# Performance work log

Measured on AMD Instinct MI355X. Metric: run time of the kernel, lower is better.

Reference implementation:

```python
import jax, jax.numpy as jnp
import numpy as np
import math

# ---- static config (must match init_kwargs / input_specs) ----
D = 1024
N_HEAD = 16
HEAD_DIM = D // N_HEAD          # 64
HALF = HEAD_DIM // 2            # rope half dim = 32
N_EXP = 8
TOP_K = 2
CAP_FACTOR = 2.0
LN_EPS = 1e-5


def _build_sin_cos(T, half_dim, dtype=jnp.float32):
    pos = jnp.arange(T, dtype=dtype)[:, None]                      # (T,1)
    inv_freq = 1.0 / (10000.0 ** (jnp.arange(0, 2 * half_dim, 2, dtype=dtype) / (2 * half_dim)))
    ang = pos * inv_freq[None, :]                                  # (T, half)
    return jnp.sin(ang), jnp.cos(ang)


def _layernorm(x, g, b):
    mu = jnp.mean(x, axis=-1, keepdims=True)
    var = jnp.mean(jnp.square(x - mu), axis=-1, keepdims=True)
    return (x - mu) * jax.lax.rsqrt(var + LN_EPS) * g + b


def _apply_rope(q, k, sin, cos):
    # q,k: (B,T,H,hd); sin,cos: (T, half)
    s = sin[None, :, None, :]
    c = cos[None, :, None, :]
    q1, q2 = q[..., :HALF], q[..., HALF:]
    k1, k2 = k[..., :HALF], k[..., HALF:]
    qr = jnp.concatenate([q1 * c - q2 * s, q1 * s + q2 * c], axis=-1)
    kr = jnp.concatenate([k1 * c - k2 * s, k1 * s + k2 * c], axis=-1)
    return qr, kr


def _attention(x, Wqkv, Wproj):
    B, T, C = x.shape
    qkv = x @ Wqkv                                                  # (B,T,3C)
    qkv = qkv.reshape(B, T, N_HEAD, 3 * HEAD_DIM)
    q, k, v = jnp.split(qkv, 3, axis=-1)                            # each (B,T,H,hd)
    sin, cos = _build_sin_cos(T, HALF)
    q, k = _apply_rope(q, k, sin, cos)
    scale = 1.0 / math.sqrt(HEAD_DIM)
    att = jnp.einsum('bqhd,bkhd->bhqk', q, k) * scale               # (B,H,T,T)
    causal = jnp.tril(jnp.ones((T, T), dtype=bool))
    att = jnp.where(causal[None, None], att, jnp.finfo(att.dtype).min)
    p = jax.nn.softmax(att, axis=-1)
    o = jnp.einsum('bhqk,bkhd->bqhd', p, v).reshape(B, T, C)
    return o @ Wproj, k, v


def _sparse_moe(flat, Wgate, W1, b1, W2, b2):
    # flat: (N, d). Eval mode: no router noise.
    N, d = flat.shape
    capacity = int(math.ceil(CAP_FACTOR * N / N_EXP))
    logits = flat @ Wgate                                           # (N,E)
    gates = jax.nn.softmax(logits, axis=-1)
    vals, inds = jax.lax.top_k(gates, TOP_K)                        # (N,k)
    flat_inds = inds.reshape(-1)                                    # (N*k,)
    flat_vals = vals.reshape(-1)
    neg = jnp.finfo(flat.dtype).min
    # per-expert assignment scores over all (token, slot) pairs
    scores = jnp.where(flat_inds[None, :] == jnp.arange(N_EXP)[:, None],
                       flat_vals[None, :], neg)                     # (E, N*k)
    top_scores, top_pos = jax.lax.top_k(scores, capacity)           # (E, cap)
    tok_idx = top_pos // TOP_K                                      # (E, cap)
    w = jnp.where(top_scores > neg, top_scores, 0.0)                # dropped slots -> 0 weight
    xe = flat[tok_idx]                                              # gather: (E, cap, d)
    h = jax.nn.gelu(jnp.einsum('ecd,edh->ech', xe, W1) + b1[:, None, :], approximate=False)
    out = jnp.einsum('ech,ehd->ecd', h, W2) + b2[:, None, :]
    out = out * w[..., None]
    final = jnp.zeros_like(flat).at[tok_idx.reshape(-1)].add(out.reshape(-1, d))
    return final


def setup_inputs() -> dict:
    key = jax.random.key(0)
    ks = jax.random.split(key, 10)
    B, T = 2, 2048
    s = 0.02
    return {
        'x': jax.random.normal(ks[0], (B, T, D), dtype=jnp.float32),
        'ln1_g': jnp.ones((D,), jnp.float32),
        'ln1_b': jnp.zeros((D,), jnp.float32),
        'ln2_g': jnp.ones((D,), jnp.float32),
        'ln2_b': jnp.zeros((D,), jnp.float32),
        'Wqkv': jax.random.normal(ks[1], (D, 3 * D), jnp.float32) * s,
        'Wproj': jax.random.normal(ks[2], (D, D), jnp.float32) * s,
        'Wgate': jax.random.normal(ks[3], (D, N_EXP), jnp.float32) * s,
        'W1': jax.random.normal(ks[4], (N_EXP, D, 4 * D), jnp.float32) * s,
        'b1': jnp.zeros((N_EXP, 4 * D), jnp.float32),
        'W2': jax.random.normal(ks[5], (N_EXP, 4 * D, D), jnp.float32) * s,
        'b2': jnp.zeros((N_EXP, D), jnp.float32),
    }


def reference(x, ln1_g, ln1_b, ln2_g, ln2_b, Wqkv, Wproj, Wgate, W1, b1, W2, b2):
    B, T, _ = x.shape
    x_norm = _layernorm(x, ln1_g, ln1_b)
    attn_out, k, v = _attention(x_norm, Wqkv, Wproj)
    x = x + attn_out
    ff_in = _layernorm(x, ln2_g, ln2_b)
    moe_out = _sparse_moe(ff_in.reshape(B * T, D), Wgate, W1, b1, W2, b2)
    x = x + moe_out.reshape(B, T, D)
    aux_loss = jnp.zeros((), x.dtype)  # eval mode
    return x, aux_loss, k, v
```

## Files before the change

### kernel.cpp

```cpp
#include <hip/hip_runtime.h>
#include <hip/hip_bf16.h>
#include <math.h>


#define TT 2048
#define NTOK 4096

typedef __attribute__((ext_vector_type(8))) short bf16x8;
typedef __attribute__((ext_vector_type(4))) float f32x4;
typedef __attribute__((ext_vector_type(16))) float f32x16;

static __device__ __forceinline__ ushort f2bf(float f) {
  union { float f; unsigned u; } v; v.f = f;
  unsigned r = v.u + 0x7FFFu + ((v.u >> 16) & 1u);
  return (ushort)(r >> 16);
}
static __device__ __forceinline__ float bf2f(ushort h) {
  union { unsigned u; float f; } v; v.u = ((unsigned)h) << 16; return v.f;
}
static __device__ __forceinline__ unsigned cvt_pk_bf16(float lo, float hi) {
  unsigned r;
  asm("v_cvt_pk_bf16_f32 %0, %1, %2" : "=v"(r) : "v"(lo), "v"(hi));
  return r;
}
static __device__ __forceinline__ void plane_swap(unsigned& a, unsigned& b) {
  asm("v_permlane32_swap_b32 %0, %1" : "+v"(a), "+v"(b));
}

__global__ __launch_bounds__(256)
void ln_kernel(const float* __restrict__ x, const float* __restrict__ g,
               const float* __restrict__ b, float* __restrict__ out) {
  int row = blockIdx.x, tid = threadIdx.x;
  const float4* xr = (const float4*)(x + (size_t)row * 1024);
  float4 v = xr[tid];
  float s = v.x + v.y + v.z + v.w;
  #pragma unroll
  for (int off = 1; off < 64; off <<= 1) s += __shfl_xor(s, off);
  __shared__ float red1[4], red2[4];
  if ((tid & 63) == 0) red1[tid >> 6] = s;
  __syncthreads();
  float mu = (red1[0] + red1[1] + red1[2] + red1[3]) * (1.0f / 1024.0f);
  float dx = v.x - mu, dy = v.y - mu, dz = v.z - mu, dw = v.w - mu;
  float ss = dx*dx + dy*dy + dz*dz + dw*dw;
  #pragma unroll
  for (int off = 1; off < 64; off <<= 1) ss += __shfl_xor(ss, off);
  if ((tid & 63) == 0) red2[tid >> 6] = ss;
  __syncthreads();
  float var = (red2[0] + red2[1] + red2[2] + red2[3]) * (1.0f / 1024.0f);
  float inv = 1.0f / sqrtf(var + 1e-5f);
  float4 g4 = ((const float4*)g)[tid];
  float4 b4 = ((const float4*)b)[tid];
  float4 o4;
  o4.x = dx * inv * g4.x + b4.x;
  o4.y = dy * inv * g4.y + b4.y;
  o4.z = dz * inv * g4.z + b4.z;
  o4.w = dw * inv * g4.w + b4.w;
  ((float4*)(out + (size_t)row * 1024))[tid] = o4;
}

__global__ void sincos_kernel(float* __restrict__ st, float* __restrict__ ct) {
  int t = blockIdx.x, j = threadIdx.x;
  double invf = pow(10000.0, -((double)(2 * j)) / 64.0);
  double ang = (double)t * invf;
  st[t * 32 + j] = (float)sin(ang);
  ct[t * 32 + j] = (float)cos(ang);
}

__global__ __launch_bounds__(256)
void rope_kernel(float* __restrict__ qkv, const float* __restrict__ st,
                 const float* __restrict__ ct, float* __restrict__ kout,
                 float* __restrict__ vout, ushort* __restrict__ Kh,
                 ushort* __restrict__ Kl) {
  int row = blockIdx.x;
  int t = row & (TT - 1);
  int b = row >> 11;
  int tid = threadIdx.x;
  float* base = qkv + (size_t)row * 3072;
  #pragma unroll
  for (int l = 0; l < 2; ++l) {
    int idx = l * 256 + tid;
    int h = idx >> 5, j = idx & 31;
    float s = st[t * 32 + j], c = ct[t * 32 + j];
    float* qp = base + h * 192;
    float q1 = qp[j], q2 = qp[j + 32];
    qp[j]      = q1 * c - q2 * s;
    qp[j + 32] = q1 * s + q2 * c;
    float k1 = qp[64 + j], k2 = qp[96 + j];
    float kr1 = k1 * c - k2 * s, kr2 = k1 * s + k2 * c;
    qp[64 + j] = kr1; qp[96 + j] = kr2;
    kout[(size_t)row * 1024 + h * 64 + j]      = kr1;
    kout[(size_t)row * 1024 + h * 64 + 32 + j] = kr2;
    size_t kb = ((size_t)(b * 16 + h) * TT + t) * 64;
    ushort h1 = f2bf(kr1);
    Kh[kb + j] = h1; Kl[kb + j] = f2bf(kr1 - bf2f(h1));
    ushort h2 = f2bf(kr2);
    Kh[kb + 32 + j] = h2; Kl[kb + 32 + j] = f2bf(kr2 - bf2f(h2));
  }
  #pragma unroll
  for (int l = 0; l < 4; ++l) {
    int f = l * 256 + tid;
    int h = f >> 6, d = f & 63;
    vout[(size_t)row * 1024 + f] = base[h * 192 + 128 + d];
  }
}

__global__ __launch_bounds__(256)
void vtprep_kernel(const float* __restrict__ vout, ushort* __restrict__ Vth,
                   ushort* __restrict__ Vtl) {
  __shared__ float tile[64][65];
  int t0 = blockIdx.x * 64, h = blockIdx.y, b = blockIdx.z;
  int tid = threadIdx.x;
  #pragma unroll
  for (int l = 0; l < 4; ++l) {
    int idx = l * 256 + tid;
    int r = idx >> 4, c4 = (idx & 15) * 4;
    *(float4*)&tile[r][c4] = *(const float4*)&vout[((size_t)(b * TT + t0 + r)) * 1024 + h * 64 + c4];
  }
  __syncthreads();
  int d = tid >> 2, ts = (tid & 3) * 16;
  union { bf16x8 v; ushort u[8]; } H0, H1, L0, L1;
  #pragma unroll
  for (int i = 0; i < 8; ++i) {
    float v0 = tile[ts + i][d];
    ushort hb0 = f2bf(v0);
    H0.u[i] = hb0; L0.u[i] = f2bf(v0 - bf2f(hb0));
    float v1 = tile[ts + 8 + i][d];
    ushort hb1 = f2bf(v1);
    H1.u[i] = hb1; L1.u[i] = f2bf(v1 - bf2f(hb1));
  }
  size_t basep = ((size_t)(b * 16 + h) * 64 + d) * TT + t0 + ts;
  *(bf16x8*)(Vth + basep) = H0.v;  *(bf16x8*)(Vth + basep + 8) = H1.v;
  *(bf16x8*)(Vtl + basep) = L0.v;  *(bf16x8*)(Vtl + basep + 8) = L1.v;
}

__global__ __launch_bounds__(256)
void flash6_kernel(const float* __restrict__ qkv, const ushort* __restrict__ Kh,
                   const ushort* __restrict__ Kl, const ushort* __restrict__ Vth,
                   const ushort* __restrict__ Vtl, float* __restrict__ Opart,
                   float* __restrict__ Mpart, float* __restrict__ Lpart) {
  int lin = blockIdx.x;
  int xcd = lin & 7, s = lin >> 3;
  int bh = xcd + 8 * (s / 40);
  int j = 39 - (s % 40);
  int qt, kc;
  if (j < 4)       { qt = j;                    kc = 0; }
  else if (j < 12) { qt = 4 + ((j - 4) >> 1);   kc = (j - 4) & 1; }
  else if (j < 24) { qt = 8 + (j - 12) / 3;     kc = (j - 12) % 3; }
  else             { qt = 12 + ((j - 24) >> 2); kc = (j - 24) & 3; }
  int slot = bh * 40 + j;
  int h = bh & 15, b = bh >> 4;
  int tid = threadIdx.x;
  int w = tid >> 6, lane = tid & 63;
  int q = lane & 31, LH = lane >> 5;
  size_t bT = (size_t)b * TT;
  int qglob0 = qt * 128 + w * 32;
  int qg = qglob0 + q;
  bf16x8 qH[4], qL[4];
  {
    const float* qp = qkv + (bT + qg) * 3072 + h * 192 + LH * 8;
    #pragma unroll
    for (int dblk = 0; dblk < 4; ++dblk) {
      float4 f0 = *(const float4*)(qp + dblk * 16);
      float4 f1 = *(const float4*)(qp + dblk * 16 + 4);
      float vals[8] = {f0.x, f0.y, f0.z, f0.w, f1.x, f1.y, f1.z, f1.w};
      union { bf16x8 v; ushort u[8]; } H, L;
      #pragma unroll
      for (int e = 0; e < 8; ++e) {
        ushort hb = f2bf(vals[e]);
        H.u[e] = hb; L.u[e] = f2bf(vals[e] - bf2f(hb));
      }
      qH[dblk] = H.v; qL[dblk] = L.v;
    }
  }
  const ushort* Kbh = Kh + (size_t)bh * TT * 64;
  const ushort* Kbl = Kl + (size_t)bh * TT * 64;
  const ushort* Vbh = Vth + (size_t)bh * 64 * TT;
  const ushort* Vbl = Vtl + (size_t)bh * 64 * TT;
  f32x16 accO0 = {}, accO1 = {};
  float m = -3.402823466e38f, lsum = 0.0f;
  int kvlo = kc * 512;
  int kvhi = min(kc * 512 + 512, qglob0 + 32);

  for (int kv0 = kvlo; kv0 < kvhi; kv0 += 32) {
    const ushort* kbh = Kbh + (size_t)(kv0 + q) * 64 + LH * 8;
    const ushort* kbl = Kbl + (size_t)(kv0 + q) * 64 + LH * 8;
    bf16x8 kAH[4], kAL[4];
    #pragma unroll
    for (int dblk = 0; dblk < 4; ++dblk) {
      kAH[dblk] = *(const bf16x8*)(kbh + dblk * 16);
      kAL[dblk] = *(const bf16x8*)(kbl + dblk * 16);
    }
    f32x16 sa = {}, sb = {};
    sa = __builtin_amdgcn_mfma_f32_32x32x16_bf16(kAH[0], qH[0], sa, 0, 0, 0);
    sb = __builtin_amdgcn_mfma_f32_32x32x16_bf16(kAH[2], qH[2], sb, 0, 0, 0);
    sa = __builtin_amdgcn_mfma_f32_32x32x16_bf16(kAH[1], qH[1], sa, 0, 0, 0);
    sb = __builtin_amdgcn_mfma_f32_32x32x16_bf16(kAH[3], qH[3], sb, 0, 0, 0);
    sa = __builtin_amdgcn_mfma_f32_32x32x16_bf16(kAH[0], qL[0], sa, 0, 0, 0);
    sb = __builtin_amdgcn_mfma_f32_32x32x16_bf16(kAH[2], qL[2], sb, 0, 0, 0);
    sa = __builtin_amdgcn_mfma_f32_32x32x16_bf16(kAH[1], qL[1], sa, 0, 0, 0);
    sb = __builtin_amdgcn_mfma_f32_32x32x16_bf16(kAH[3], qL[3], sb, 0, 0, 0);
    sa = __builtin_amdgcn_mfma_f32_32x32x16_bf16(kAL[0], qH[0], sa, 0, 0, 0);
    sb = __builtin_amdgcn_mfma_f32_32x32x16_bf16(kAL[2], qH[2], sb, 0, 0, 0);
    sa = __builtin_amdgcn_mfma_f32_32x32x16_bf16(kAL[1], qH[1], sa, 0, 0, 0);
    sb = __builtin_amdgcn_mfma_f32_32x32x16_bf16(kAL[3], qH[3], sb, 0, 0, 0);
    bf16x8 vAH[2][2], vAL[2][2];
    #pragma unroll
    for (int dblk = 0; dblk < 2; ++dblk)
      #pragma unroll
      for (int s2 = 0; s2 < 2; ++s2) {
        size_t ad = (size_t)(dblk * 32 + q) * TT + kv0 + s2 * 16 + LH * 8;
        vAH[dblk][s2] = *(const bf16x8*)(Vbh + ad);
        vAL[dblk][s2] = *(const bf16x8*)(Vbl + ad);
      }
    float p[16];
    float pmax = -3.402823466e38f;
    if (kv0 + 31 > qglob0) {
      #pragma unroll
      for (int r = 0; r < 16; ++r) {
        int kvg = kv0 + (r & 3) + 8 * (r >> 2) + 4 * LH;
        float sv = (kvg <= qg) ? (sa[r] + sb[r]) * 0.125f : -3.402823466e38f;
        p[r] = sv; pmax = fmaxf(pmax, sv);
      }
    } else {
      #pragma unroll
      for (int r = 0; r < 16; ++r) {
        float sv = (sa[r] + sb[r]) * 0.125f;
        p[r] = sv; pmax = fmaxf(pmax, sv);
      }
    }
    pmax = fmaxf(pmax, __shfl_xor(pmax, 32));
    float mnew = fmaxf(m, pmax);
    float fsc = __expf(m - mnew);
    float psum = 0.0f;
    #pragma unroll
    for (int r = 0; r < 16; ++r) { p[r] = __expf(p[r] - mnew); psum += p[r]; }
    psum += __shfl_xor(psum, 32);
    lsum = lsum * fsc + psum;
    m = mnew;
    #pragma unroll
    for (int r = 0; r < 16; ++r) { accO0[r] *= fsc; accO1[r] *= fsc; }
    bf16x8 pHf[2], pLf[2];
    #pragma unroll
    for (int s2 = 0; s2 < 2; ++s2) {
      int s8 = s2 * 8;
      unsigned a  = cvt_pk_bf16(p[s8 + 0], p[s8 + 1]);
      unsigned bw = cvt_pk_bf16(p[s8 + 2], p[s8 + 3]);
      unsigned c  = cvt_pk_bf16(p[s8 + 4], p[s8 + 5]);
      unsigned d  = cvt_pk_bf16(p[s8 + 6], p[s8 + 7]);
      float l0 = p[s8 + 0] - __uint_as_float(a << 16);
      float l1 = p[s8 + 1] - __uint_as_float(a & 0xFFFF0000u);
      float l2 = p[s8 + 2] - __uint_as_float(bw << 16);
      float l3 = p[s8 + 3] - __uint_as_float(bw & 0xFFFF0000u);
      float l4 = p[s8 + 4] - __uint_as_float(c << 16);
      float l5 = p[s8 + 5] - __uint_as_float(c & 0xFFFF0000u);
      float l6 = p[s8 + 6] - __uint_as_float(d << 16);
      float l7 = p[s8 + 7] - __uint_as_float(d & 0xFFFF0000u);
      unsigned al = cvt_pk_bf16(l0, l1);
      unsigned bl = cvt_pk_bf16(l2, l3);
      unsigned cl = cvt_pk_bf16(l4, l5);
      unsigned dl = cvt_pk_bf16(l6, l7);
      plane_swap(a, c); plane_swap(bw, d);
      plane_swap(al, cl); plane_swap(bl, dl);
      union { unsigned w[4]; bf16x8 v; } PH, PL;
      PH.w[0] = a;  PH.w[1] = bw; PH.w[2] = c;  PH.w[3] = d;
      PL.w[0] = al; PL.w[1] = bl; PL.w[2] = cl; PL.w[3] = dl;
      pHf[s2] = PH.v; pLf[s2] = PL.v;
    }
    #pragma unroll
    for (int s2 = 0; s2 < 2; ++s2) {
      accO0 = __builtin_amdgcn_mfma_f32_32x32x16_bf16(vAH[0][s2], pHf[s2], accO0, 0, 0, 0);
      accO1 = __builtin_amdgcn_mfma_f32_32x32x16_bf16(vAH[1][s2], pHf[s2], accO1, 0, 0, 0);
      accO0 = __builtin_amdgcn_mfma_f32_32x32x16_bf16(vAH[0][s2], pLf[s2], accO0, 0, 0, 0);
      accO1 = __builtin_amdgcn_mfma_f32_32x32x16_bf16(vAH[1][s2], pLf[s2], accO1, 0, 0, 0);
      accO0 = __builtin_amdgcn_mfma_f32_32x32x16_bf16(vAL[0][s2], pHf[s2], accO0, 0, 0, 0);
      accO1 = __builtin_amdgcn_mfma_f32_32x32x16_bf16(vAL[1][s2], pHf[s2], accO1, 0, 0, 0);
    }
  }
  if (LH == 0) {
    Mpart[slot * 128 + w * 32 + q] = m;
    Lpart[slot * 128 + w * 32 + q] = lsum;
  }
  float* Ob = Opart + (size_t)slot * 8192 + (w * 32 + q) * 64;
  #pragma unroll
  for (int g2 = 0; g2 < 4; ++g2) {
    float4 v0 = {accO0[g2 * 4 + 0], accO0[g2 * 4 + 1], accO0[g2 * 4 + 2], accO0[g2 * 4 + 3]};
    *(float4*)(Ob + 8 * g2 + 4 * LH) = v0;
    float4 v1 = {accO1[g2 * 4 + 0], accO1[g2 * 4 + 1], accO1[g2 * 4 + 2], accO1[g2 * 4 + 3]};
    *(float4*)(Ob + 32 + 8 * g2 + 4 * LH) = v1;
  }
}

__global__ __launch_bounds__(256)
void fmerge2_kernel(const float* __restrict__ Opart, const float* __restrict__ Mpart,
                    const float* __restrict__ Lpart, float* __restrict__ o) {
  int qt = blockIdx.x, bh = blockIdx.y;
  int h = bh & 15, b = bh >> 4;
  int g = qt >> 2;
  int nc = g + 1;
  int off = 2 * g * (g + 1) + (qt & 3) * (g + 1);
  int slot0 = bh * 40 + off;
  int tid = threadIdx.x;
  int q = tid & 127, dh = tid >> 7;
  float mg = -3.402823466e38f;
  for (int c = 0; c < nc; ++c) mg = fmaxf(mg, Mpart[(slot0 + c) * 128 + q]);
  float lg = 0.0f;
  float4 acc[8] = {};
  for (int c = 0; c < nc; ++c) {
    float sc = __expf(Mpart[(slot0 + c) * 128 + q] - mg);
    lg += sc * Lpart[(slot0 + c) * 128 + q];
    const float4* op = (const float4*)(Opart + (size_t)(slot0 + c) * 8192 + q * 64 + dh * 32);
    #pragma unroll
    for (int i = 0; i < 8; ++i) {
      float4 v = op[i];
      acc[i].x += sc * v.x; acc[i].y += sc * v.y;
      acc[i].z += sc * v.z; acc[i].w += sc * v.w;
    }
  }
  float inv = 1.0f / lg;
  float* ob = o + ((size_t)(b * TT + qt * 128 + q)) * 1024 + h * 64 + dh * 32;
  #pragma unroll
  for (int i = 0; i < 8; ++i) {
    float4 v = {acc[i].x * inv, acc[i].y * inv, acc[i].z * inv, acc[i].w * inv};
    *(float4*)(ob + i * 4) = v;
  }
}

template<bool LO>
__global__ void tconv_kernel(const float* __restrict__ in, ushort* __restrict__ oh,
                             ushort* __restrict__ ol, int K, int N) {
  __shared__ float t[32][33];
  int z = blockIdx.z;
  const float* ip = in + (size_t)z * K * N;
  ushort* ohp = oh + (size_t)z * K * N;
  ushort* olp = LO ? (ol + (size_t)z * K * N) : nullptr;
  int n0 = blockIdx.x * 32, k0 = blockIdx.y * 32;
  int tx = threadIdx.x, ty = threadIdx.y;
  #pragma unroll
  for (int i = 0; i < 4; ++i)
    t[ty + 8 * i][tx] = ip[(size_t)(k0 + ty + 8 * i) * N + n0 + tx];
  __syncthreads();
  #pragma unroll
  for (int i = 0; i < 4; ++i) {
    float v = t[tx][ty + 8 * i];
    size_t off = (size_t)(n0 + ty + 8 * i) * K + k0 + tx;
    ushort hb = f2bf(v);
    ohp[off] = hb;
    if (LO) olp[off] = f2bf(v - bf2f(hb));
  }
}

__global__ __launch_bounds__(256)
void split_kernel(const float* __restrict__ in, ushort* __restrict__ oh,
                  ushort* __restrict__ ol) {
  size_t i = ((size_t)blockIdx.x * 256 + threadIdx.x) * 4;
  float4 v = *(const float4*)(in + i);
  ushort h0 = f2bf(v.x), h1 = f2bf(v.y), h2 = f2bf(v.z), h3 = f2bf(v.w);
  ushort4 hh = {h0, h1, h2, h3};
  *(ushort4*)(oh + i) = hh;
  ushort4 ll = {f2bf(v.x - bf2f(h0)), f2bf(v.y - bf2f(h1)),
                f2bf(v.z - bf2f(h2)), f2bf(v.w - bf2f(h3))};
  *(ushort4*)(ol + i) = ll;
}

#define LOAD_STEP(tt) do {                                                     \
    int seg = SPLIT3 ? ((tt) / kPer) : 0;                                      \
    int kk = (SPLIT3 ? ((tt) % kPer) : (tt)) << 6;                             \
    const ushort* Ause = (SPLIT3 && seg == 2) ? AlB : AhB;                     \
    const ushort* Buse = (SPLIT3 && seg == 1) ? BlB : BhB;                     \
    _Pragma("unroll")                                                          \
    for (int q = 0; q < 4; ++q) {                                              \
      int rr = r0 + 32 * q;                                                    \
      int clog = cph ^ (rr & 7);                                               \
      ra[q] = *(const bf16x8*)(Ause + (size_t)garow[q] * K + kk + clog * 8);   \
      rb[q] = *(const bf16x8*)(Buse + (size_t)(bn + rr) * K + kk + clog * 8);  \
    }                                                                          \
  } while (0)

template<int EPI, bool GATHER, bool SPLIT3>
__global__ __launch_bounds__(256, 2)
void mgemm(const ushort* __restrict__ Ah, const ushort* __restrict__ Al,
           const ushort* __restrict__ Bh, const ushort* __restrict__ Bl,
           void* __restrict__ Cv, const float* __restrict__ extra,
           const int* __restrict__ gatAll, int N, int K,
           long aEStride, long bEStride, long cEStride, int biasEStride) {
  __shared__ ushort As[128 * 64];
  __shared__ ushort Bs[128 * 64];
  int z = blockIdx.z;
  const ushort* AhB = Ah + (size_t)z * aEStride;
  const ushort* AlB = SPLIT3 ? (Al + (size_t)z * aEStride) : nullptr;
  const ushort* BhB = Bh + (size_t)z * bEStride;
  const ushort* BlB = SPLIT3 ? (Bl + (size_t)z * bEStride) : nullptr;
  const int* gat = GATHER ? (gatAll + z * 1024) : nullptr;
  int bm = blockIdx.y * 128, bn = blockIdx.x * 128;
  int tid = threadIdx.x;
  int r0 = tid >> 3, cph = tid & 7;
  int garow[4];
  #pragma unroll
  for (int q = 0; q < 4; ++q) {
    int rr = r0 + 32 * q;
    garow[q] = GATHER ? gat[bm + rr] : (bm + rr);
  }
  int kPer = K >> 6;
  int kSteps = (SPLIT3 ? 3 : 1) * kPer;
  int wid = tid >> 6, lane = tid & 63;
  int wm = wid >> 1, wn = wid & 1;
  int lr = lane & 15, lk = lane >> 4;
  f32x4 acc[4][4] = {};
  bf16x8 ra[4], rb[4];
  LOAD_STEP(0);
  for (int t = 0; t < kSteps; ++t) {
    __syncthreads();
    #pragma unroll
    for (int q = 0; q < 4; ++q) {
      int rr = r0 + 32 * q;
      *(bf16x8*)&As[rr * 64 + cph * 8] = ra[q];
      *(bf16x8*)&Bs[rr * 64 + cph * 8] = rb[q];
    }
    __syncthreads();
    if (t + 1 < kSteps) LOAD_STEP(t + 1);
    #pragma unroll
    for (int kh = 0; kh < 2; ++kh) {
      bf16x8 af[4], bfr[4];
      #pragma unroll
      for (int mf = 0; mf < 4; ++mf) {
        int row = wm * 64 + mf * 16 + lr;
        int ch = (kh * 4 + lk) ^ (row & 7);
        af[mf] = *(const bf16x8*)&As[row * 64 + ch * 8];
      }
      #pragma unroll
      for (int nf = 0; nf < 4; ++nf) {
        int row = wn * 64 + nf * 16 + lr;
        int ch = (kh * 4 + lk) ^ (row & 7);
        bfr[nf] = *(const bf16x8*)&Bs[row * 64 + ch * 8];
      }
      #pragma unroll
      for (int mf = 0; mf < 4; ++mf)
        #pragma unroll
        for (int nf = 0; nf < 4; ++nf)
          acc[mf][nf] = __builtin_amdgcn_mfma_f32_16x16x32_bf16(af[mf], bfr[nf], acc[mf][nf], 0, 0, 0);
    }
  }
  int crow = bm + wm * 64, ccol = bn + wn * 64;
  if constexpr (EPI <= 1) {
    float* C = (float*)Cv;
    #pragma unroll
    for (int mf = 0; mf < 4; ++mf)
      #pragma unroll
      for (int nf = 0; nf < 4; ++nf)
        #pragma unroll
        for (int r = 0; r < 4; ++r) {
          int row = crow + mf * 16 + lk * 4 + r;
          int col = ccol + nf * 16 + lr;
          float v = acc[mf][nf][r];
          if constexpr (EPI == 1) v += extra[(size_t)row * N + col];
          C[(size_t)row * N + col] = v;
        }
  } else {
    const float* bias = extra + (size_t)z * biasEStride;
    ushort* C = (ushort*)Cv + (size_t)z * cEStride;
    #pragma unroll
    for (int mf = 0; mf < 4; ++mf)
      #pragma unroll
      for (int nf = 0; nf < 4; ++nf)
        #pragma unroll
        for (int r = 0; r < 4; ++r) {
          int row = crow + mf * 16 + lk * 4 + r;
          int col = ccol + nf * 16 + lr;
          float v = acc[mf][nf][r] + bias[col];
          if constexpr (EPI == 2)
            v = 0.5f * v * (1.0f + erff(v * 0.70710678118654752f));
          C[(size_t)row * N + col] = f2bf(v);
        }
  }
}

__global__ __launch_bounds__(256)
void gate_kernel(const float* __restrict__ ffin, const float* __restrict__ Wg,
                 int* __restrict__ te, float* __restrict__ tv, int* __restrict__ inv) {
  int token = blockIdx.x, tid = threadIdx.x;
  float acc[8] = {};
  const float* xr = ffin + (size_t)token * 1024;
  for (int i = tid; i < 1024; i += 256) {
    float xv = xr[i];
    const float4* wr = (const float4*)&Wg[i * 8];
    float4 w0 = wr[0], w1 = wr[1];
    acc[0] += xv * w0.x; acc[1] += xv * w0.y; acc[2] += xv * w0.z; acc[3] += xv * w0.w;
    acc[4] += xv * w1.x; acc[5] += xv * w1.y; acc[6] += xv * w1.z; acc[7] += xv * w1.w;
  }
  #pragma unroll
  for (int off = 1; off < 64; off <<= 1)
    #pragma unroll
    for (int q = 0; q < 8; ++q) acc[q] += __shfl_xor(acc[q], off);
  __shared__ float red[4][8];
  if ((tid & 63) == 0)
    #pragma unroll
    for (int q = 0; q < 8; ++q) red[tid >> 6][q] = acc[q];
  __syncthreads();
  if (tid == 0) {
    float g[8];
    #pragma unroll
    for (int q = 0; q < 8; ++q) g[q] = red[0][q] + red[1][q] + red[2][q] + red[3][q];
    float mx = g[0];
    #pragma unroll
    for (int q = 1; q < 8; ++q) mx = fmaxf(mx, g[q]);
    float sum = 0.0f;
    #pragma unroll
    for (int q = 0; q < 8; ++q) { g[q] = expf(g[q] - mx); sum += g[q]; }
    float inv_s = 1.0f / sum;
    #pragma unroll
    for (int q = 0; q < 8; ++q) g[q] *= inv_s;
    int e1 = 0; float v1 = g[0];
    for (int q = 1; q < 8; ++q) if (g[q] > v1) { v1 = g[q]; e1 = q; }
    int e2 = -1; float v2 = -1.0f;
    for (int q = 0; q < 8; ++q) { if (q == e1) continue; if (g[q] > v2) { v2 = g[q]; e2 = q; } }
    te[token * 2] = e1; te[token * 2 + 1] = e2;
    tv[token * 2] = v1; tv[token * 2 + 1] = v2;
    inv[token * 2] = -1; inv[token * 2 + 1] = -1;
  }
}

__global__ __launch_bounds__(1024)
void route_sort_kernel(const int* __restrict__ te, const float* __restrict__ tv,
                       int* __restrict__ etok, float* __restrict__ ew,
                       int* __restrict__ inv) {
  __shared__ unsigned long long sk[4096];
  __shared__ int wcnt[16];
  __shared__ int base;
  int e = blockIdx.x, tid = threadIdx.x;
  int lane = tid & 63, wv = tid >> 6;
  if (tid == 0) base = 0;
  __syncthreads();
  for (int c = 0; c < 8; ++c) {
    int s = c * 1024 + tid;
    bool sel = (te[s] == e);
    unsigned long long ball = __ballot(sel);
    int pre = __popcll(ball & ((1ull << lane) - 1ull));
    if (lane == 0) wcnt[wv] = __popcll(ball);
    __syncthreads();
    int woff = 0, tot = 0;
    #pragma unroll
    for (int i = 0; i < 16; ++i) {
      int cc = wcnt[i];
      if (i < wv) woff += cc;
      tot += cc;
    }
    if (sel) {
      unsigned vb = __float_as_uint(tv[s]);
      sk[base + woff + pre] =
          ((unsigned long long)vb << 32) | (unsigned)(0xFFFFFFFFu - (unsigned)s);
    }
    __syncthreads();
    if (tid == 0) base += tot;
    __syncthreads();
  }
  int n = base;
  if (n > 1024) {
    int P = (n <= 2048) ? 2048 : 4096;
    for (int i = n + tid; i < P; i += 1024) sk[i] = 0ull;
    __syncthreads();
    for (int k = 2; k <= P; k <<= 1)
      for (int j = k >> 1; j > 0; j >>= 1) {
        for (int t = tid; t < (P >> 1); t += 1024) {
          int i = ((t & ~(j - 1)) << 1) | (t & (j - 1));
          int p = i | j;
          unsigned long long a = sk[i], bq = sk[p];
          bool desc = ((i & k) == 0);
          if (desc ? (a < bq) : (a > bq)) { sk[i] = bq; sk[p] = a; }
        }
        __syncthreads();
      }
  }
  int cap = n < 1024 ? n : 1024;
  if (tid < cap) {
    unsigned long long key = sk[tid];
    unsigned slot = 0xFFFFFFFFu - (unsigned)(key & 0xFFFFFFFFull);
    etok[e * 1024 + tid] = (int)(slot >> 1);
    ew[e * 1024 + tid] = __uint_as_float((unsigned)(key >> 32));
    inv[slot] = e * 1024 + tid;
  } else {
    etok[e * 1024 + tid] = 0;
    ew[e * 1024 + tid] = 0.0f;
  }
}

__global__ __launch_bounds__(256)
void combine_kernel(const float* __restrict__ xres, const ushort* __restrict__ eo,
                    const int* __restrict__ inv, const float* __restrict__ ew,
                    float* __restrict__ outx, float* __restrict__ aux) {
  int token = blockIdx.x;
  int d = threadIdx.x * 4;
  float4 acc = *(const float4*)&xres[(size_t)token * 1024 + d];
  #pragma unroll
  for (int j = 0; j < 2; ++j) {
    int p = inv[token * 2 + j];
    if (p >= 0) {
      float w = ew[p];
      const ushort* ep = eo + (size_t)p * 1024 + d;
      acc.x += w * bf2f(ep[0]); acc.y += w * bf2f(ep[1]);
      acc.z += w * bf2f(ep[2]); acc.w += w * bf2f(ep[3]);
    }
  }
  *(float4*)&outx[(size_t)token * 1024 + d] = acc;
  if (token == 0 && threadIdx.x == 0) aux[0] = 0.0f;
}

extern "C" void kernel_launch(void* const* d_in, const int* in_sizes, int n_in,
                              void* d_out, int out_size, void* d_ws, size_t ws_size,
                              hipStream_t stream) {
  const float* x     = (const float*)d_in[0];
  const float* ln1g  = (const float*)d_in[1];
  const float* ln1b  = (const float*)d_in[2];
  const float* ln2g  = (const float*)d_in[3];
  const float* ln2b  = (const float*)d_in[4];
  const float* Wqkv  = (const float*)d_in[5];
  const float* Wproj = (const float*)d_in[6];
  const float* Wg    = (const float*)d_in[7];
  const float* W1    = (const float*)d_in[8];
  const float* b1    = (const float*)d_in[9];
  const float* W2    = (const float*)d_in[10];
  const float* b2    = (const float*)d_in[11];

  float* out_x   = (float*)d_out;
  float* out_aux = out_x + 4194304;
  float* out_k   = out_aux + 1;
  float* out_v   = out_k + 4194304;

  float* ws   = (float*)d_ws;
  float* A    = ws;
  float* qkvb = ws + 4194304;
  float* o    = ws + 16777216;
  float* st   = ws + 20971520;
  float* ct   = ws + 21037056;
  int*   te   = (int*)(ws + 21102592);
  float* tv   = ws + 21110784;
  int*   etok = (int*)(ws + 21118976);
  float* ew   = ws + 21127168;
  int*   inv  = (int*)(ws + 21135360);
  ushort* bfAh = (ushort*)(ws + 21143552);
  ushort* bfAl = (ushort*)(ws + 23240704);
  ushort* BqH  = (ushort*)(ws + 25337856);
  ushort* BqL  = (ushort*)(ws + 26910720);
  ushort* BpH  = (ushort*)(ws + 28483584);
  ushort* BpL  = (ushort*)(ws + 29007872);
  ushort* W1t  = (ushort*)(ws + 29532160);
  ushort* W2t  = (ushort*)(ws + 46309376);
  ushort* eo   = (ushort*)(ws + 63086592);
  ushort* hbuf = (ushort*)(ws + 4194304);
  ushort* Kh_  = bfAh;
  ushort* Kl_  = bfAl;
  ushort* Vth_ = eo;
  ushort* Vtl_ = eo + 4194304;
  float* Opart = ws + 29532160;
  float* Mpart = ws + 40017920;
  float* Lpart = ws + 40181760;

  tconv_kernel<true ><<<dim3(96, 32, 1),  dim3(32, 8), 0, stream>>>(Wqkv,  BqH, BqL, 1024, 3072);
  tconv_kernel<true ><<<dim3(32, 32, 1),  dim3(32, 8), 0, stream>>>(Wproj, BpH, BpL, 1024, 1024);
  sincos_kernel<<<TT, 32, 0, stream>>>(st, ct);

  ln_kernel<<<NTOK, 256, 0, stream>>>(x, ln1g, ln1b, A);
  split_kernel<<<4096, 256, 0, stream>>>(A, bfAh, bfAl);
  mgemm<0, false, true><<<dim3(24, 32, 1), 256, 0, stream>>>(
      bfAh, bfAl, BqH, BqL, qkvb, nullptr, nullptr, 3072, 1024, 0, 0, 0, 0);
  rope_kernel<<<NTOK, 256, 0, stream>>>(qkvb, st, ct, out_k, out_v, Kh_, Kl_);
  vtprep_kernel<<<dim3(32, 16, 2), 256, 0, stream>>>(out_v, Vth_, Vtl_);
  flash6_kernel<<<1280, 256, 0, stream>>>(qkvb, Kh_, Kl_, Vth_, Vtl_, Opart, Mpart, Lpart);
  fmerge2_kernel<<<dim3(16, 32), 256, 0, stream>>>(Opart, Mpart, Lpart, o);
  split_kernel<<<4096, 256, 0, stream>>>(o, bfAh, bfAl);
  mgemm<1, false, true><<<dim3(8, 32, 1), 256, 0, stream>>>(
      bfAh, bfAl, BpH, BpL, A, x, nullptr, 1024, 1024, 0, 0, 0, 0);
  tconv_kernel<false><<<dim3(128, 32, 8), dim3(32, 8), 0, stream>>>(W1, W1t, nullptr, 1024, 4096);
  tconv_kernel<false><<<dim3(32, 128, 8), dim3(32, 8), 0, stream>>>(W2, W2t, nullptr, 4096, 1024);
  ln_kernel<<<NTOK, 256, 0, stream>>>(A, ln2g, ln2b, o);
  gate_kernel<<<NTOK, 256, 0, stream>>>(o, Wg, te, tv, inv);
  split_kernel<<<4096, 256, 0, stream>>>(o, bfAh, bfAl);
  route_sort_kernel<<<8, 1024, 0, stream>>>(te, tv, etok, ew, inv);
  mgemm<2, true, false><<<dim3(32, 8, 8), 256, 0, stream>>>(
      bfAh, nullptr, W1t, nullptr, hbuf, b1, etok, 4096, 1024,
      0, 4096L * 1024, 1024L * 4096, 4096);
  mgemm<3, false, false><<<dim3(8, 8, 8), 256, 0, stream>>>(
      hbuf, nullptr, W2t, nullptr, eo, b2, nullptr, 1024, 4096,
      1024L * 4096, 1024L * 4096, 1024L * 1024, 1024);
  combine_kernel<<<NTOK, 256, 0, stream>>>(A, eo, inv, ew, out_x, out_aux);
}
```

Baseline: 699.3 us.

## Fuse bf16 hi/lo split into producers and load GEMM tiles directly to LDS

Removes the three separate split kernels by having the layernorm and flash-merge kernels write bf16 hi/lo pairs directly, which drops an fp32 round trip through global memory for each one. Separately, the mgemm kernel now uses global_load_lds to copy A/B tiles straight into shared memory in place of register staging. The register-prefetch of the next k-step is gone, so global-load latency is no longer overlapped with MFMA work within a block. Overlap now depends on the second resident block per CU.

After: 711.5 us. Within noise of the previous version (+1.7%).

```diff
diff --git a/kernel.cpp b/kernel.cpp
--- a/kernel.cpp
+++ b/kernel.cpp
@@ -26,10 +26,17 @@
 static __device__ __forceinline__ void plane_swap(unsigned& a, unsigned& b) {
   asm("v_permlane32_swap_b32 %0, %1" : "+v"(a), "+v"(b));
 }
-
+static __device__ __forceinline__ void gload16(const void* g, void* l) {
+  __builtin_amdgcn_global_load_lds(
+      (const __attribute__((address_space(1))) void*)g,
+      (__attribute__((address_space(3))) void*)l, 16, 0, 0);
+}
+
+template<bool WF32>
 __global__ __launch_bounds__(256)
 void ln_kernel(const float* __restrict__ x, const float* __restrict__ g,
-               const float* __restrict__ b, float* __restrict__ out) {
+               const float* __restrict__ b, float* __restrict__ out,
+               ushort* __restrict__ oh, ushort* __restrict__ ol) {
   int row = blockIdx.x, tid = threadIdx.x;
   const float4* xr = (const float4*)(x + (size_t)row * 1024);
   float4 v = xr[tid];
@@ -55,7 +62,15 @@
   o4.y = dy * inv * g4.y + b4.y;
   o4.z = dz * inv * g4.z + b4.z;
   o4.w = dw * inv * g4.w + b4.w;
-  ((float4*)(out + (size_t)row * 1024))[tid] = o4;
+  if constexpr (WF32)
+    ((float4*)(out + (size_t)row * 1024))[tid] = o4;
+  size_t base = (size_t)row * 1024 + tid * 4;
+  ushort h0 = f2bf(o4.x), h1 = f2bf(o4.y), h2 = f2bf(o4.z), h3 = f2bf(o4.w);
+  ushort4 hh = {h0, h1, h2, h3};
+  *(ushort4*)(oh + base) = hh;
+  ushort4 ll = {f2bf(o4.x - bf2f(h0)), f2bf(o4.y - bf2f(h1)),
+                f2bf(o4.z - bf2f(h2)), f2bf(o4.w - bf2f(h3))};
+  *(ushort4*)(ol + base) = ll;
 }
 
 __global__ void sincos_kernel(float* __restrict__ st, float* __restrict__ ct) {
@@ -292,7 +307,8 @@
 
 __global__ __launch_bounds__(256)
 void fmerge2_kernel(const float* __restrict__ Opart, const float* __restrict__ Mpart,
-                    const float* __restrict__ Lpart, float* __restrict__ o) {
+                    const float* __restrict__ Lpart, ushort* __restrict__ oh,
+                    ushort* __restrict__ ol) {
   int qt = blockIdx.x, bh = blockIdx.y;
   int h = bh & 15, b = bh >> 4;
   int g = qt >> 2;
@@ -317,11 +333,16 @@
     }
   }
   float inv = 1.0f / lg;
-  float* ob = o + ((size_t)(b * TT + qt * 128 + q)) * 1024 + h * 64 + dh * 32;
+  size_t obase = ((size_t)(b * TT + qt * 128 + q)) * 1024 + h * 64 + dh * 32;
   #pragma unroll
   for (int i = 0; i < 8; ++i) {
     float4 v = {acc[i].x * inv, acc[i].y * inv, acc[i].z * inv, acc[i].w * inv};
-    *(float4*)(ob + i * 4) = v;
+    ushort h0 = f2bf(v.x), h1 = f2bf(v.y), h2 = f2bf(v.z), h3 = f2bf(v.w);
+    ushort4 hh = {h0, h1, h2, h3};
+    *(ushort4*)(oh + obase + i * 4) = hh;
+    ushort4 ll = {f2bf(v.x - bf2f(h0)), f2bf(v.y - bf2f(h1)),
+                  f2bf(v.z - bf2f(h2)), f2bf(v.w - bf2f(h3))};
+    *(ushort4*)(ol + obase + i * 4) = ll;
   }
 }
 
@@ -348,33 +369,6 @@
     if (LO) olp[off] = f2bf(v - bf2f(hb));
   }
 }
-
-__global__ __launch_bounds__(256)
-void split_kernel(const float* __restrict__ in, ushort* __restrict__ oh,
-                  ushort* __restrict__ ol) {
-  size_t i = ((size_t)blockIdx.x * 256 + threadIdx.x) * 4;
-  float4 v = *(const float4*)(in + i);
-  ushort h0 = f2bf(v.x), h1 = f2bf(v.y), h2 = f2bf(v.z), h3 = f2bf(v.w);
-  ushort4 hh = {h0, h1, h2, h3};
-  *(ushort4*)(oh + i) = hh;
-  ushort4 ll = {f2bf(v.x - bf2f(h0)), f2bf(v.y - bf2f(h1)),
-                f2bf(v.z - bf2f(h2)), f2bf(v.w - bf2f(h3))};
-  *(ushort4*)(ol + i) = ll;
-}
-
-#define LOAD_STEP(tt) do {                                                     \
-    int seg = SPLIT3 ? ((tt) / kPer) : 0;                                      \
-    int kk = (SPLIT3 ? ((tt) % kPer) : (tt)) << 6;                             \
-    const ushort* Ause = (SPLIT3 && seg == 2) ? AlB : AhB;                     \
-    const ushort* Buse = (SPLIT3 && seg == 1) ? BlB : BhB;                     \
-    _Pragma("unroll")                                                          \
-    for (int q = 0; q < 4; ++q) {                                              \
-      int rr = r0 + 32 * q;                                                    \
-      int clog = cph ^ (rr & 7);                                               \
-      ra[q] = *(const bf16x8*)(Ause + (size_t)garow[q] * K + kk + clog * 8);   \
-      rb[q] = *(const bf16x8*)(Buse + (size_t)(bn + rr) * K + kk + clog * 8);  \
-    }                                                                          \
-  } while (0)
 
 template<int EPI, bool GATHER, bool SPLIT3>
 __global__ __launch_bounds__(256, 2)
@@ -393,31 +387,35 @@
   const int* gat = GATHER ? (gatAll + z * 1024) : nullptr;
   int bm = blockIdx.y * 128, bn = blockIdx.x * 128;
   int tid = threadIdx.x;
-  int r0 = tid >> 3, cph = tid & 7;
+  int wid = tid >> 6, lane = tid & 63;
+  int w32 = wid * 32;
+  int lrow = lane >> 3, cph = lane & 7;
   int garow[4];
   #pragma unroll
-  for (int q = 0; q < 4; ++q) {
-    int rr = r0 + 32 * q;
-    garow[q] = GATHER ? gat[bm + rr] : (bm + rr);
+  for (int i = 0; i < 4; ++i) {
+    int row = w32 + i * 8 + lrow;
+    garow[i] = GATHER ? gat[bm + row] : (bm + row);
   }
   int kPer = K >> 6;
   int kSteps = (SPLIT3 ? 3 : 1) * kPer;
-  int wid = tid >> 6, lane = tid & 63;
   int wm = wid >> 1, wn = wid & 1;
   int lr = lane & 15, lk = lane >> 4;
   f32x4 acc[4][4] = {};
-  bf16x8 ra[4], rb[4];
-  LOAD_STEP(0);
+
   for (int t = 0; t < kSteps; ++t) {
+    int seg = SPLIT3 ? (t / kPer) : 0;
+    int kk = (SPLIT3 ? (t % kPer) : t) << 6;
+    const ushort* Ause = (SPLIT3 && seg == 2) ? AlB : AhB;
+    const ushort* Buse = (SPLIT3 && seg == 1) ? BlB : BhB;
     __syncthreads();
     #pragma unroll
-    for (int q = 0; q < 4; ++q) {
-      int rr = r0 + 32 * q;
-      *(bf16x8*)&As[rr * 64 + cph * 8] = ra[q];
-      *(bf16x8*)&Bs[rr * 64 + cph * 8] = rb[q];
+    for (int i = 0; i < 4; ++i) {
+      int row = w32 + i * 8 + lrow;
+      int sc = cph ^ (row & 7);
+      gload16(Ause + (size_t)garow[i] * K + kk + sc * 8, As + (w32 + i * 8) * 64);
+      gload16(Buse + (size_t)(bn + row) * K + kk + sc * 8, Bs + (w32 + i * 8) * 64);
     }
     __syncthreads();
-    if (t + 1 < kSteps) LOAD_STEP(t + 1);
     #pragma unroll
     for (int kh = 0; kh < 2; ++kh) {
       bf16x8 af[4], bfr[4];
@@ -658,22 +656,19 @@
   tconv_kernel<true ><<<dim3(32, 32, 1),  dim3(32, 8), 0, stream>>>(Wproj, BpH, BpL, 1024, 1024);
   sincos_kernel<<<TT, 32, 0, stream>>>(st, ct);
 
-  ln_kernel<<<NTOK, 256, 0, stream>>>(x, ln1g, ln1b, A);
-  split_kernel<<<4096, 256, 0, stream>>>(A, bfAh, bfAl);
+  ln_kernel<false><<<NTOK, 256, 0, stream>>>(x, ln1g, ln1b, nullptr, bfAh, bfAl);
   mgemm<0, false, true><<<dim3(24, 32, 1), 256, 0, stream>>>(
       bfAh, bfAl, BqH, BqL, qkvb, nullptr, nullptr, 3072, 1024, 0, 0, 0, 0);
   rope_kernel<<<NTOK, 256, 0, stream>>>(qkvb, st, ct, out_k, out_v, Kh_, Kl_);
   vtprep_kernel<<<dim3(32, 16, 2), 256, 0, stream>>>(out_v, Vth_, Vtl_);
   flash6_kernel<<<1280, 256, 0, stream>>>(qkvb, Kh_, Kl_, Vth_, Vtl_, Opart, Mpart, Lpart);
-  fmerge2_kernel<<<dim3(16, 32), 256, 0, stream>>>(Opart, Mpart, Lpart, o);
-  split_kernel<<<4096, 256, 0, stream>>>(o, bfAh, bfAl);
+  fmerge2_kernel<<<dim3(16, 32), 256, 0, stream>>>(Opart, Mpart, Lpart, bfAh, bfAl);
   mgemm<1, false, true><<<dim3(8, 32, 1), 256, 0, stream>>>(
       bfAh, bfAl, BpH, BpL, A, x, nullptr, 1024, 1024, 0, 0, 0, 0);
   tconv_kernel<false><<<dim3(128, 32, 8), dim3(32, 8), 0, stream>>>(W1, W1t, nullptr, 1024, 4096);
   tconv_kernel<false><<<dim3(32, 128, 8), dim3(32, 8), 0, stream>>>(W2, W2t, nullptr, 4096, 1024);
-  ln_kernel<<<NTOK, 256, 0, stream>>>(A, ln2g, ln2b, o);
+  ln_kernel<true><<<NTOK, 256, 0, stream>>>(A, ln2g, ln2b, o, bfAh, bfAl);
   gate_kernel<<<NTOK, 256, 0, stream>>>(o, Wg, te, tv, inv);
-  split_kernel<<<4096, 256, 0, stream>>>(o, bfAh, bfAl);
   route_sort_kernel<<<8, 1024, 0, stream>>>(te, tv, etok, ew, inv);
   mgemm<2, true, false><<<dim3(32, 8, 8), 256, 0, stream>>>(
       bfAh, nullptr, W1t, nullptr, hbuf, b1, etok, 4096, 1024,
```

## Fuse bf16 hi/lo split into layernorm and merge; finer flash KV chunks

Applied to the files above, without the earlier changes.

Removes the three standalone split kernels by having the layernorm kernels and the flash merge kernel write bf16 hi/lo pairs directly, which saves fp32 round trips through memory and three launches. The flash attention kernel now splits KV into 256-wide chunks (72 work items per batch-head instead of 40) for finer load balance, and the merge kernel is updated to match. It also raises wave priority around the MFMA blocks with s_setprio. The cost is more partial outputs to merge and a larger Opart/Mpart/Lpart footprint, so the workspace offsets are moved.

Result: no change. 704.0 us (+0.7%).

```diff
diff --git a/kernel.cpp b/kernel.cpp
--- a/kernel.cpp
+++ b/kernel.cpp
@@ -27,9 +27,11 @@
   asm("v_permlane32_swap_b32 %0, %1" : "+v"(a), "+v"(b));
 }
 
+template<bool WF32>
 __global__ __launch_bounds__(256)
 void ln_kernel(const float* __restrict__ x, const float* __restrict__ g,
-               const float* __restrict__ b, float* __restrict__ out) {
+               const float* __restrict__ b, float* __restrict__ out,
+               ushort* __restrict__ oh, ushort* __restrict__ ol) {
   int row = blockIdx.x, tid = threadIdx.x;
   const float4* xr = (const float4*)(x + (size_t)row * 1024);
   float4 v = xr[tid];
@@ -55,7 +57,15 @@
   o4.y = dy * inv * g4.y + b4.y;
   o4.z = dz * inv * g4.z + b4.z;
   o4.w = dw * inv * g4.w + b4.w;
-  ((float4*)(out + (size_t)row * 1024))[tid] = o4;
+  if constexpr (WF32)
+    ((float4*)(out + (size_t)row * 1024))[tid] = o4;
+  size_t base = (size_t)row * 1024 + tid * 4;
+  ushort h0 = f2bf(o4.x), h1 = f2bf(o4.y), h2 = f2bf(o4.z), h3 = f2bf(o4.w);
+  ushort4 hh = {h0, h1, h2, h3};
+  *(ushort4*)(oh + base) = hh;
+  ushort4 ll = {f2bf(o4.x - bf2f(h0)), f2bf(o4.y - bf2f(h1)),
+                f2bf(o4.z - bf2f(h2)), f2bf(o4.w - bf2f(h3))};
+  *(ushort4*)(ol + base) = ll;
 }
 
 __global__ void sincos_kernel(float* __restrict__ st, float* __restrict__ ct) {
@@ -134,20 +144,21 @@
 }
 
 __global__ __launch_bounds__(256)
-void flash6_kernel(const float* __restrict__ qkv, const ushort* __restrict__ Kh,
+void flash7_kernel(const float* __restrict__ qkv, const ushort* __restrict__ Kh,
                    const ushort* __restrict__ Kl, const ushort* __restrict__ Vth,
                    const ushort* __restrict__ Vtl, float* __restrict__ Opart,
                    float* __restrict__ Mpart, float* __restrict__ Lpart) {
+  const int offt[16] = {0,1,2,4,6,9,12,16,20,25,30,36,42,49,56,64};
   int lin = blockIdx.x;
   int xcd = lin & 7, s = lin >> 3;
-  int bh = xcd + 8 * (s / 40);
-  int j = 39 - (s % 40);
-  int qt, kc;
-  if (j < 4)       { qt = j;                    kc = 0; }
-  else if (j < 12) { qt = 4 + ((j - 4) >> 1);   kc = (j - 4) & 1; }
-  else if (j < 24) { qt = 8 + (j - 12) / 3;     kc = (j - 12) % 3; }
-  else             { qt = 12 + ((j - 24) >> 2); kc = (j - 24) & 3; }
-  int slot = bh * 40 + j;
+  int bh = xcd + 8 * (s / 72);
+  int j = 71 - (s % 72);
+  int qt = 0, off = 0;
+  #pragma unroll
+  for (int u = 0; u < 16; ++u)
+    if (j >= offt[u]) { qt = u; off = offt[u]; }
+  int kc = j - off;
+  int slot = bh * 72 + j;
   int h = bh & 15, b = bh >> 4;
   int tid = threadIdx.x;
   int w = tid >> 6, lane = tid & 63;
@@ -178,8 +189,8 @@
   const ushort* Vbl = Vtl + (size_t)bh * 64 * TT;
   f32x16 accO0 = {}, accO1 = {};
   float m = -3.402823466e38f, lsum = 0.0f;
-  int kvlo = kc * 512;
-  int kvhi = min(kc * 512 + 512, qglob0 + 32);
+  int kvlo = kc * 256;
+  int kvhi = min(kvlo + 256, qglob0 + 32);
 
   for (int kv0 = kvlo; kv0 < kvhi; kv0 += 32) {
     const ushort* kbh = Kbh + (size_t)(kv0 + q) * 64 + LH * 8;
@@ -191,6 +202,7 @@
       kAL[dblk] = *(const bf16x8*)(kbl + dblk * 16);
     }
     f32x16 sa = {}, sb = {};
+    __builtin_amdgcn_s_setprio(1);
     sa = __builtin_amdgcn_mfma_f32_32x32x16_bf16(kAH[0], qH[0], sa, 0, 0, 0);
     sb = __builtin_amdgcn_mfma_f32_32x32x16_bf16(kAH[2], qH[2], sb, 0, 0, 0);
     sa = __builtin_amdgcn_mfma_f32_32x32x16_bf16(kAH[1], qH[1], sa, 0, 0, 0);
@@ -203,6 +215,7 @@
     sb = __builtin_amdgcn_mfma_f32_32x32x16_bf16(kAL[2], qH[2], sb, 0, 0, 0);
     sa = __builtin_amdgcn_mfma_f32_32x32x16_bf16(kAL[1], qH[1], sa, 0, 0, 0);
     sb = __builtin_amdgcn_mfma_f32_32x32x16_bf16(kAL[3], qH[3], sb, 0, 0, 0);
+    __builtin_amdgcn_s_setprio(0);
     bf16x8 vAH[2][2], vAL[2][2];
     #pragma unroll
     for (int dblk = 0; dblk < 2; ++dblk)
@@ -266,6 +279,7 @@
       PL.w[0] = al; PL.w[1] = bl; PL.w[2] = cl; PL.w[3] = dl;
       pHf[s2] = PH.v; pLf[s2] = PL.v;
     }
+    __builtin_amdgcn_s_setprio(1);
     #pragma unroll
     for (int s2 = 0; s2 < 2; ++s2) {
       accO0 = __builtin_amdgcn_mfma_f32_32x32x16_bf16(vAH[0][s2], pHf[s2], accO0, 0, 0, 0);
@@ -275,6 +289,7 @@
       accO0 = __builtin_amdgcn_mfma_f32_32x32x16_bf16(vAL[0][s2], pHf[s2], accO0, 0, 0, 0);
       accO1 = __builtin_amdgcn_mfma_f32_32x32x16_bf16(vAL[1][s2], pHf[s2], accO1, 0, 0, 0);
     }
+    __builtin_amdgcn_s_setprio(0);
   }
   if (LH == 0) {
     Mpart[slot * 128 + w * 32 + q] = m;
@@ -292,13 +307,13 @@
 
 __global__ __launch_bounds__(256)
 void fmerge2_kernel(const float* __restrict__ Opart, const float* __restrict__ Mpart,
-                    const float* __restrict__ Lpart, float* __restrict__ o) {
+                    const float* __restrict__ Lpart, ushort* __restrict__ oh,
+                    ushort* __restrict__ ol) {
+  const int offt[16] = {0,1,2,4,6,9,12,16,20,25,30,36,42,49,56,64};
   int qt = blockIdx.x, bh = blockIdx.y;
   int h = bh & 15, b = bh >> 4;
-  int g = qt >> 2;
-  int nc = g + 1;
-  int off = 2 * g * (g + 1) + (qt & 3) * (g + 1);
-  int slot0 = bh * 40 + off;
+  int nc = (qt + 2) >> 1;
+  int slot0 = bh * 72 + offt[qt];
   int tid = threadIdx.x;
   int q = tid & 127, dh = tid >> 7;
   float mg = -3.402823466e38f;
@@ -317,11 +332,16 @@
     }
   }
   float inv = 1.0f / lg;
-  float* ob = o + ((size_t)(b * TT + qt * 128 + q)) * 1024 + h * 64 + dh * 32;
+  size_t obase = ((size_t)(b * TT + qt * 128 + q)) * 1024 + h * 64 + dh * 32;
   #pragma unroll
   for (int i = 0; i < 8; ++i) {
     float4 v = {acc[i].x * inv, acc[i].y * inv, acc[i].z * inv, acc[i].w * inv};
-    *(float4*)(ob + i * 4) = v;
+    ushort h0 = f2bf(v.x), h1 = f2bf(v.y), h2 = f2bf(v.z), h3 = f2bf(v.w);
+    ushort4 hh = {h0, h1, h2, h3};
+    *(ushort4*)(oh + obase + i * 4) = hh;
+    ushort4 ll = {f2bf(v.x - bf2f(h0)), f2bf(v.y - bf2f(h1)),
+                  f2bf(v.z - bf2f(h2)), f2bf(v.w - bf2f(h3))};
+    *(ushort4*)(ol + obase + i * 4) = ll;
   }
 }
 
@@ -347,19 +367,6 @@
     ohp[off] = hb;
     if (LO) olp[off] = f2bf(v - bf2f(hb));
   }
-}
-
-__global__ __launch_bounds__(256)
-void split_kernel(const float* __restrict__ in, ushort* __restrict__ oh,
-                  ushort* __restrict__ ol) {
-  size_t i = ((size_t)blockIdx.x * 256 + threadIdx.x) * 4;
-  float4 v = *(const float4*)(in + i);
-  ushort h0 = f2bf(v.x), h1 = f2bf(v.y), h2 = f2bf(v.z), h3 = f2bf(v.w);
-  ushort4 hh = {h0, h1, h2, h3};
-  *(ushort4*)(oh + i) = hh;
-  ushort4 ll = {f2bf(v.x - bf2f(h0)), f2bf(v.y - bf2f(h1)),
-                f2bf(v.z - bf2f(h2)), f2bf(v.w - bf2f(h3))};
-  *(ushort4*)(ol + i) = ll;
 }
 
 #define LOAD_STEP(tt) do {                                                     \
@@ -651,29 +658,26 @@
   ushort* Vth_ = eo;
   ushort* Vtl_ = eo + 4194304;
   float* Opart = ws + 29532160;
-  float* Mpart = ws + 40017920;
-  float* Lpart = ws + 40181760;
+  float* Mpart = ws + 48406528;
+  float* Lpart = ws + 48701440;
 
   tconv_kernel<true ><<<dim3(96, 32, 1),  dim3(32, 8), 0, stream>>>(Wqkv,  BqH, BqL, 1024, 3072);
   tconv_kernel<true ><<<dim3(32, 32, 1),  dim3(32, 8), 0, stream>>>(Wproj, BpH, BpL, 1024, 1024);
   sincos_kernel<<<TT, 32, 0, stream>>>(st, ct);
 
-  ln_kernel<<<NTOK, 256, 0, stream>>>(x, ln1g, ln1b, A);
-  split_kernel<<<4096, 256, 0, stream>>>(A, bfAh, bfAl);
+  ln_kernel<false><<<NTOK, 256, 0, stream>>>(x, ln1g, ln1b, nullptr, bfAh, bfAl);
   mgemm<0, false, true><<<dim3(24, 32, 1), 256, 0, stream>>>(
       bfAh, bfAl, BqH, BqL, qkvb, nullptr, nullptr, 3072, 1024, 0, 0, 0, 0);
   rope_kernel<<<NTOK, 256, 0, stream>>>(qkvb, st, ct, out_k, out_v, Kh_, Kl_);
   vtprep_kernel<<<dim3(32, 16, 2), 256, 0, stream>>>(out_v, Vth_, Vtl_);
-  flash6_kernel<<<1280, 256, 0, stream>>>(qkvb, Kh_, Kl_, Vth_, Vtl_, Opart, Mpart, Lpart);
-  fmerge2_kernel<<<dim3(16, 32), 256, 0, stream>>>(Opart, Mpart, Lpart, o);
-  split_kernel<<<4096, 256, 0, stream>>>(o, bfAh, bfAl);
+  flash7_kernel<<<2304, 256, 0, stream>>>(qkvb, Kh_, Kl_, Vth_, Vtl_, Opart, Mpart, Lpart);
+  fmerge2_kernel<<<dim3(16, 32), 256, 0, stream>>>(Opart, Mpart, Lpart, bfAh, bfAl);
   mgemm<1, false, true><<<dim3(8, 32, 1), 256, 0, stream>>>(
       bfAh, bfAl, BpH, BpL, A, x, nullptr, 1024, 1024, 0, 0, 0, 0);
   tconv_kernel<false><<<dim3(128, 32, 8), dim3(32, 8), 0, stream>>>(W1, W1t, nullptr, 1024, 4096);
   tconv_kernel<false><<<dim3(32, 128, 8), dim3(32, 8), 0, stream>>>(W2, W2t, nullptr, 4096, 1024);
-  ln_kernel<<<NTOK, 256, 0, stream>>>(A, ln2g, ln2b, o);
+  ln_kernel<true><<<NTOK, 256, 0, stream>>>(A, ln2g, ln2b, o, bfAh, bfAl);
   gate_kernel<<<NTOK, 256, 0, stream>>>(o, Wg, te, tv, inv);
-  split_kernel<<<4096, 256, 0, stream>>>(o, bfAh, bfAl);
   route_sort_kernel<<<8, 1024, 0, stream>>>(te, tv, etok, ew, inv);
   mgemm<2, true, false><<<dim3(32, 8, 8), 256, 0, stream>>>(
       bfAh, nullptr, W1t, nullptr, hbuf, b1, etok, 4096, 1024,
```
